# Performance work log

Measured on AMD Instinct MI355X. Metric: run time of the kernel, lower is better.

## Reference

```python
import jax, jax.numpy as jnp
import numpy as np
from jax import lax

B, C, H, W = 128, 256, 32, 32
KH, KW = 8, 8


def depthwise_xcorr(x, kernel):
    """Depthwise cross-correlation: each (batch, channel) plane of x is
    correlated with the matching (batch, channel) plane of kernel,
    equivalent to F.conv2d(x.view(1,B*C,H,W), k.view(B*C,1,kh,kw), groups=B*C).
    Note torch conv2d is cross-correlation (no kernel flip), matching lax."""
    b, c, h, w = x.shape
    kh, kw = kernel.shape[2], kernel.shape[3]
    xr = x.reshape(1, b * c, h, w)
    kr = kernel.reshape(b * c, 1, kh, kw)
    out = lax.conv_general_dilated(
        xr, kr,
        window_strides=(1, 1),
        padding='VALID',
        dimension_numbers=('NCHW', 'OIHW', 'NCHW'),
        feature_group_count=b * c,
    )  # (1, b*c, h-kh+1, w-kw+1)
    return out.reshape(b, c, h - kh + 1, w - kw + 1)


def setup_inputs() -> dict:
    key = jax.random.key(0)
    k1, k2 = jax.random.split(key)
    x = jax.random.normal(k1, (B, C, H, W), dtype=jnp.float32)
    kernel = jax.random.normal(k2, (B, C, KH, KW), dtype=jnp.float32)
    weight = jnp.ones((3,), dtype=jnp.float32)  # nn.Parameter(torch.ones(channels))
    return {"x": x, "kernel": kernel, "weight": weight}


def reference(x, kernel, weight):
    # Original runs three identical depthwise-correlation implementations
    # (testCon2dSvf, testCon2dPSvf, F.conv2d) over the same data, then blends
    # with softmax weights. Since all three compute the same correlation,
    # out = (w0 + w1 + w2) * corr. We compute the correlation once.
    corr = depthwise_xcorr(x, kernel)
    w = jax.nn.softmax(weight, axis=0)
    return (w[0] + w[1] + w[2]) * corr
```

## Files before the change

### kernel.cpp

```cpp
#include <hip/hip_runtime.h>


#define NPLANES (128 * 256)
#define PPB 8
#define RST 18
#define XP  592
#define KTB (PPB * XP)
#define KTS 36
#define LDS_DW (KTB + PPB * KTS)
#define OH 25
#define OW 25

__device__ __forceinline__ unsigned cvt_pk_bf16(float a, float b) {
    unsigned r;
    asm("v_cvt_pk_bf16_f32 %0, %1, %2" : "=v"(r) : "v"(a), "v"(b));
    return r;
}
__device__ __forceinline__ void dot2(float& acc, unsigned x2, unsigned k2) {
    asm("v_dot2_f32_bf16 %0, %1, %2, %0" : "+v"(acc) : "v"(x2), "v"(k2));
}
__device__ __forceinline__ unsigned alignb(unsigned hi, unsigned lo, unsigned sh) {
    unsigned r;
    asm("v_alignbit_b32 %0, %1, %2, %3" : "=v"(r) : "v"(hi), "v"(lo), "v"(sh));
    return r;
}

__device__ __forceinline__ int plane_shift(int pl) {
    const int m = pl % 3;
    return (m == 0) ? 0 : (m == 1) ? 12 : 8;
}

__global__ __launch_bounds__(256)
void dwxcorr_kernel(const float* __restrict__ x,
                    const float* __restrict__ kern,
                    float* __restrict__ out) {
    __shared__ unsigned ldsu[LDS_DW];
    const int tid = threadIdx.x;
    const int plane0 = blockIdx.x * PPB;

#pragma unroll
    for (int it = 0; it < 2; ++it) {
        const int u    = tid + it * 256;
        const int pl   = u >> 6;
        const int rh   = u & 63;
        const int row  = rh >> 1;
        const int half = rh & 1;
        const float* g = x + (size_t)(plane0 + pl) * 1024 + row * 32 + half * 16;
        const float4 v0 = *reinterpret_cast<const float4*>(g + 0);
        const float4 v1 = *reinterpret_cast<const float4*>(g + 4);
        const float4 v2 = *reinterpret_cast<const float4*>(g + 8);
        const float4 v3 = *reinterpret_cast<const float4*>(g + 12);
        unsigned A[8];
        A[0] = cvt_pk_bf16(v0.x, v0.y); A[1] = cvt_pk_bf16(v0.z, v0.w);
        A[2] = cvt_pk_bf16(v1.x, v1.y); A[3] = cvt_pk_bf16(v1.z, v1.w);
        A[4] = cvt_pk_bf16(v2.x, v2.y); A[5] = cvt_pk_bf16(v2.z, v2.w);
        A[6] = cvt_pk_bf16(v3.x, v3.y); A[7] = cvt_pk_bf16(v3.z, v3.w);
        unsigned* base = &ldsu[pl * XP + plane_shift(pl) + row * RST + half * 8];
        *reinterpret_cast<uint2*>(base + 0) = make_uint2(A[0], A[1]);
        *reinterpret_cast<uint2*>(base + 2) = make_uint2(A[2], A[3]);
        *reinterpret_cast<uint2*>(base + 4) = make_uint2(A[4], A[5]);
        *reinterpret_cast<uint2*>(base + 6) = make_uint2(A[6], A[7]);
    }
    if (tid < PPB * 16) {
        const int pl = tid >> 4;
        const int o4 = tid & 15;
        const float4 v =
            *reinterpret_cast<const float4*>(kern + (size_t)(plane0 + pl) * 64 + o4 * 4);
        unsigned* kb = &ldsu[KTB + pl * KTS + o4 * 2];
        kb[0] = cvt_pk_bf16(v.x, v.y);
        kb[1] = cvt_pk_bf16(v.z, v.w);
    }
    __syncthreads();

    const int pb = tid / 25;
    if (pb >= PPB) return;
    const int ox = tid % 25;

    unsigned kt[32];
    {
        const unsigned* kp = &ldsu[KTB + pb * KTS];
#pragma unroll
        for (int i = 0; i < 8; ++i) {
            const uint4 q = *reinterpret_cast<const uint4*>(kp + 4 * i);
            kt[4*i+0] = q.x; kt[4*i+1] = q.y; kt[4*i+2] = q.z; kt[4*i+3] = q.w;
        }
    }

    float acc[OH];
#pragma unroll
    for (int i = 0; i < OH; ++i) acc[i] = 0.f;

    const unsigned sh = (ox & 1) * 16;
    const unsigned* xb = &ldsu[pb * XP + plane_shift(pb) + (ox >> 1)];
#pragma unroll
    for (int r = 0; r < 32; ++r) {
        const unsigned* rp = xb + r * RST;
        const unsigned d0 = rp[0], d1 = rp[1], d2 = rp[2], d3 = rp[3], d4 = rp[4];
        const unsigned w0 = alignb(d1, d0, sh);
        const unsigned w1 = alignb(d2, d1, sh);
        const unsigned w2 = alignb(d3, d2, sh);
        const unsigned w3 = alignb(d4, d3, sh);
#pragma unroll
        for (int ky = 0; ky < 8; ++ky) {
            const int oy = r - ky;
            if (oy >= 0 && oy < OH) {
                dot2(acc[oy], w0, kt[ky * 4 + 0]);
                dot2(acc[oy], w1, kt[ky * 4 + 1]);
                dot2(acc[oy], w2, kt[ky * 4 + 2]);
                dot2(acc[oy], w3, kt[ky * 4 + 3]);
            }
        }
    }

    float* op = out + (size_t)(plane0 + pb) * (OH * OW) + ox;
#pragma unroll
    for (int oy = 0; oy < OH; ++oy) op[oy * OW] = acc[oy];
}

extern "C" void kernel_launch(void* const* d_in, const int* in_sizes, int n_in,
                              void* d_out, int out_size, void* d_ws, size_t ws_size,
                              hipStream_t stream) {
    const float* x = (const float*)d_in[0];
    const float* k = (const float*)d_in[1];
    float* out = (float*)d_out;
    const int nblocks = NPLANES / PPB;
    dwxcorr_kernel<<<nblocks, 256, 0, stream>>>(x, k, out);
}
```

Before: 43.84 us.

## Compute two output columns per thread and halve block size to 128

Each thread now computes an even and an odd output column from the same loaded LDS words. The even column uses the raw bf16 pairs and the odd column uses a fixed 16-bit funnel shift, which removes the per-thread variable shift and halves the LDS row reads per output. The block shrinks to 128 threads, with 104 active in compute, so the staging loop doubles its iterations. This doubles the accumulator registers (50 floats plus 32 kernel values) and cuts the number of active threads per plane, which risks lower occupancy and less latency hiding.

```diff
diff --git a/kernel.cpp b/kernel.cpp
--- a/kernel.cpp
+++ b/kernel.cpp
@@ -19,9 +19,9 @@
 __device__ __forceinline__ void dot2(float& acc, unsigned x2, unsigned k2) {
     asm("v_dot2_f32_bf16 %0, %1, %2, %0" : "+v"(acc) : "v"(x2), "v"(k2));
 }
-__device__ __forceinline__ unsigned alignb(unsigned hi, unsigned lo, unsigned sh) {
+__device__ __forceinline__ unsigned funnel16(unsigned hi, unsigned lo) {
     unsigned r;
-    asm("v_alignbit_b32 %0, %1, %2, %3" : "=v"(r) : "v"(hi), "v"(lo), "v"(sh));
+    asm("v_alignbit_b32 %0, %1, %2, 16" : "=v"(r) : "v"(hi), "v"(lo));
     return r;
 }
 
@@ -30,7 +30,7 @@
     return (m == 0) ? 0 : (m == 1) ? 12 : 8;
 }
 
-__global__ __launch_bounds__(256)
+__global__ __launch_bounds__(128)
 void dwxcorr_kernel(const float* __restrict__ x,
                     const float* __restrict__ kern,
                     float* __restrict__ out) {
@@ -39,8 +39,8 @@
     const int plane0 = blockIdx.x * PPB;
 
 #pragma unroll
-    for (int it = 0; it < 2; ++it) {
-        const int u    = tid + it * 256;
+    for (int it = 0; it < 4; ++it) {
+        const int u    = tid + it * 128;
         const int pl   = u >> 6;
         const int rh   = u & 63;
         const int row  = rh >> 1;
@@ -61,7 +61,7 @@
         *reinterpret_cast<uint2*>(base + 4) = make_uint2(A[4], A[5]);
         *reinterpret_cast<uint2*>(base + 6) = make_uint2(A[6], A[7]);
     }
-    if (tid < PPB * 16) {
+    {
         const int pl = tid >> 4;
         const int o4 = tid & 15;
         const float4 v =
@@ -72,9 +72,9 @@
     }
     __syncthreads();
 
-    const int pb = tid / 25;
-    if (pb >= PPB) return;
-    const int ox = tid % 25;
+    if (tid >= PPB * 13) return;
+    const int pb = tid / 13;
+    const int j  = tid - pb * 13;
 
     unsigned kt[32];
     {
@@ -85,36 +85,46 @@
             kt[4*i+0] = q.x; kt[4*i+1] = q.y; kt[4*i+2] = q.z; kt[4*i+3] = q.w;
         }
     }
+#pragma unroll
+    for (int i = 0; i < 32; ++i)
+        asm volatile("" : "+v"(kt[i]));
 
-    float acc[OH];
+    float accE[OH], accO[OH];
 #pragma unroll
-    for (int i = 0; i < OH; ++i) acc[i] = 0.f;
+    for (int i = 0; i < OH; ++i) { accE[i] = 0.f; accO[i] = 0.f; }
 
-    const unsigned sh = (ox & 1) * 16;
-    const unsigned* xb = &ldsu[pb * XP + plane_shift(pb) + (ox >> 1)];
+    const unsigned* xb = &ldsu[pb * XP + plane_shift(pb) + j];
 #pragma unroll
     for (int r = 0; r < 32; ++r) {
         const unsigned* rp = xb + r * RST;
         const unsigned d0 = rp[0], d1 = rp[1], d2 = rp[2], d3 = rp[3], d4 = rp[4];
-        const unsigned w0 = alignb(d1, d0, sh);
-        const unsigned w1 = alignb(d2, d1, sh);
-        const unsigned w2 = alignb(d3, d2, sh);
-        const unsigned w3 = alignb(d4, d3, sh);
+        const unsigned v0 = funnel16(d1, d0);
+        const unsigned v1 = funnel16(d2, d1);
+        const unsigned v2 = funnel16(d3, d2);
+        const unsigned v3 = funnel16(d4, d3);
 #pragma unroll
         for (int ky = 0; ky < 8; ++ky) {
             const int oy = r - ky;
             if (oy >= 0 && oy < OH) {
-                dot2(acc[oy], w0, kt[ky * 4 + 0]);
-                dot2(acc[oy], w1, kt[ky * 4 + 1]);
-                dot2(acc[oy], w2, kt[ky * 4 + 2]);
-                dot2(acc[oy], w3, kt[ky * 4 + 3]);
+                dot2(accE[oy], d0, kt[ky * 4 + 0]);
+                dot2(accE[oy], d1, kt[ky * 4 + 1]);
+                dot2(accE[oy], d2, kt[ky * 4 + 2]);
+                dot2(accE[oy], d3, kt[ky * 4 + 3]);
+                dot2(accO[oy], v0, kt[ky * 4 + 0]);
+                dot2(accO[oy], v1, kt[ky * 4 + 1]);
+                dot2(accO[oy], v2, kt[ky * 4 + 2]);
+                dot2(accO[oy], v3, kt[ky * 4 + 3]);
             }
         }
     }
 
-    float* op = out + (size_t)(plane0 + pb) * (OH * OW) + ox;
+    float* op = out + (size_t)(plane0 + pb) * (OH * OW);
+    const int c0 = 2 * j;
 #pragma unroll
-    for (int oy = 0; oy < OH; ++oy) op[oy * OW] = acc[oy];
+    for (int oy = 0; oy < OH; ++oy) {
+        op[oy * OW + c0] = accE[oy];
+        if (c0 + 1 < OW) op[oy * OW + c0 + 1] = accO[oy];
+    }
 }
 
 extern "C" void kernel_launch(void* const* d_in, const int* in_sizes, int n_in,
@@ -124,5 +134,5 @@
     const float* k = (const float*)d_in[1];
     float* out = (float*)d_out;
     const int nblocks = NPLANES / PPB;
-    dwxcorr_kernel<<<nblocks, 256, 0, stream>>>(x, k, out);
+    dwxcorr_kernel<<<nblocks, 128, 0, stream>>>(x, k, out);
 }
```

Result: slower. 45.77 us (+4.4%).

## Split input staging into two halves to overlap second-half loads with compute

Applied to the files above, without the earlier changes.

Each thread now stages only the top 16 rows of every plane into LDS before the first barrier. It issues the global loads for the bottom 16 rows, then computes the first 16 rows of correlation, and only afterwards converts and stores the second half before a second barrier. The aim is to hide global-load latency behind the dot2 compute of the first half. In exchange it adds a second __syncthreads and holds 16 extra float registers across the compute phase, which could reduce occupancy.

```diff
diff --git a/kernel.cpp b/kernel.cpp
--- a/kernel.cpp
+++ b/kernel.cpp
@@ -30,6 +30,21 @@
     return (m == 0) ? 0 : (m == 1) ? 12 : 8;
 }
 
+__device__ __forceinline__ void pack_store_half(unsigned* ldsu, int pl, int row,
+                                                int half, float4 v0, float4 v1,
+                                                float4 v2, float4 v3) {
+    unsigned A[8];
+    A[0] = cvt_pk_bf16(v0.x, v0.y); A[1] = cvt_pk_bf16(v0.z, v0.w);
+    A[2] = cvt_pk_bf16(v1.x, v1.y); A[3] = cvt_pk_bf16(v1.z, v1.w);
+    A[4] = cvt_pk_bf16(v2.x, v2.y); A[5] = cvt_pk_bf16(v2.z, v2.w);
+    A[6] = cvt_pk_bf16(v3.x, v3.y); A[7] = cvt_pk_bf16(v3.z, v3.w);
+    unsigned* base = &ldsu[pl * XP + plane_shift(pl) + row * RST + half * 8];
+    *reinterpret_cast<uint2*>(base + 0) = make_uint2(A[0], A[1]);
+    *reinterpret_cast<uint2*>(base + 2) = make_uint2(A[2], A[3]);
+    *reinterpret_cast<uint2*>(base + 4) = make_uint2(A[4], A[5]);
+    *reinterpret_cast<uint2*>(base + 6) = make_uint2(A[6], A[7]);
+}
+
 __global__ __launch_bounds__(256)
 void dwxcorr_kernel(const float* __restrict__ x,
                     const float* __restrict__ kern,
@@ -38,28 +53,18 @@
     const int tid = threadIdx.x;
     const int plane0 = blockIdx.x * PPB;
 
-#pragma unroll
-    for (int it = 0; it < 2; ++it) {
-        const int u    = tid + it * 256;
-        const int pl   = u >> 6;
-        const int rh   = u & 63;
-        const int row  = rh >> 1;
-        const int half = rh & 1;
-        const float* g = x + (size_t)(plane0 + pl) * 1024 + row * 32 + half * 16;
+    const int upl  = tid >> 5;
+    const int urh  = tid & 31;
+    const int urow = urh >> 1;
+    const int uhalf = urh & 1;
+
+    {
+        const float* g = x + (size_t)(plane0 + upl) * 1024 + urow * 32 + uhalf * 16;
         const float4 v0 = *reinterpret_cast<const float4*>(g + 0);
         const float4 v1 = *reinterpret_cast<const float4*>(g + 4);
         const float4 v2 = *reinterpret_cast<const float4*>(g + 8);
         const float4 v3 = *reinterpret_cast<const float4*>(g + 12);
-        unsigned A[8];
-        A[0] = cvt_pk_bf16(v0.x, v0.y); A[1] = cvt_pk_bf16(v0.z, v0.w);
-        A[2] = cvt_pk_bf16(v1.x, v1.y); A[3] = cvt_pk_bf16(v1.z, v1.w);
-        A[4] = cvt_pk_bf16(v2.x, v2.y); A[5] = cvt_pk_bf16(v2.z, v2.w);
-        A[6] = cvt_pk_bf16(v3.x, v3.y); A[7] = cvt_pk_bf16(v3.z, v3.w);
-        unsigned* base = &ldsu[pl * XP + plane_shift(pl) + row * RST + half * 8];
-        *reinterpret_cast<uint2*>(base + 0) = make_uint2(A[0], A[1]);
-        *reinterpret_cast<uint2*>(base + 2) = make_uint2(A[2], A[3]);
-        *reinterpret_cast<uint2*>(base + 4) = make_uint2(A[4], A[5]);
-        *reinterpret_cast<uint2*>(base + 6) = make_uint2(A[6], A[7]);
+        pack_store_half(ldsu, upl, urow, uhalf, v0, v1, v2, v3);
     }
     if (tid < PPB * 16) {
         const int pl = tid >> 4;
@@ -72,28 +77,63 @@
     }
     __syncthreads();
 
-    const int pb = tid / 25;
-    if (pb >= PPB) return;
-    const int ox = tid % 25;
+    float4 b0, b1, b2, b3;
+    {
+        const float* g =
+            x + (size_t)(plane0 + upl) * 1024 + (16 + urow) * 32 + uhalf * 16;
+        b0 = *reinterpret_cast<const float4*>(g + 0);
+        b1 = *reinterpret_cast<const float4*>(g + 4);
+        b2 = *reinterpret_cast<const float4*>(g + 8);
+        b3 = *reinterpret_cast<const float4*>(g + 12);
+    }
+
+    const bool isc = (tid < PPB * 25);
+    const int pb = isc ? (tid / 25) : 0;
+    const int ox = isc ? (tid % 25) : 0;
 
     unsigned kt[32];
-    {
+    float acc[OH];
+    const unsigned sh = (ox & 1) * 16;
+    const unsigned* xb = &ldsu[pb * XP + plane_shift(pb) + (ox >> 1)];
+
+    if (isc) {
         const unsigned* kp = &ldsu[KTB + pb * KTS];
 #pragma unroll
         for (int i = 0; i < 8; ++i) {
             const uint4 q = *reinterpret_cast<const uint4*>(kp + 4 * i);
             kt[4*i+0] = q.x; kt[4*i+1] = q.y; kt[4*i+2] = q.z; kt[4*i+3] = q.w;
         }
+#pragma unroll
+        for (int i = 0; i < OH; ++i) acc[i] = 0.f;
+
+#pragma unroll
+        for (int r = 0; r < 16; ++r) {
+            const unsigned* rp = xb + r * RST;
+            const unsigned d0 = rp[0], d1 = rp[1], d2 = rp[2], d3 = rp[3], d4 = rp[4];
+            const unsigned w0 = alignb(d1, d0, sh);
+            const unsigned w1 = alignb(d2, d1, sh);
+            const unsigned w2 = alignb(d3, d2, sh);
+            const unsigned w3 = alignb(d4, d3, sh);
+#pragma unroll
+            for (int ky = 0; ky < 8; ++ky) {
+                const int oy = r - ky;
+                if (oy >= 0) {
+                    dot2(acc[oy], w0, kt[ky * 4 + 0]);
+                    dot2(acc[oy], w1, kt[ky * 4 + 1]);
+                    dot2(acc[oy], w2, kt[ky * 4 + 2]);
+                    dot2(acc[oy], w3, kt[ky * 4 + 3]);
+                }
+            }
+        }
     }
 
-    float acc[OH];
+    pack_store_half(ldsu, upl, 16 + urow, uhalf, b0, b1, b2, b3);
+    __syncthreads();
+
+    if (!isc) return;
+
 #pragma unroll
-    for (int i = 0; i < OH; ++i) acc[i] = 0.f;
-
-    const unsigned sh = (ox & 1) * 16;
-    const unsigned* xb = &ldsu[pb * XP + plane_shift(pb) + (ox >> 1)];
-#pragma unroll
-    for (int r = 0; r < 32; ++r) {
+    for (int r = 16; r < 32; ++r) {
         const unsigned* rp = xb + r * RST;
         const unsigned d0 = rp[0], d1 = rp[1], d2 = rp[2], d3 = rp[3], d4 = rp[4];
         const unsigned w0 = alignb(d1, d0, sh);
@@ -103,7 +143,7 @@
 #pragma unroll
         for (int ky = 0; ky < 8; ++ky) {
             const int oy = r - ky;
-            if (oy >= 0 && oy < OH) {
+            if (oy < OH) {
                 dot2(acc[oy], w0, kt[ky * 4 + 0]);
                 dot2(acc[oy], w1, kt[ky * 4 + 1]);
                 dot2(acc[oy], w2, kt[ky * 4 + 2]);
```

Measured after the change: 44.64 us. About the same (+1.8%).
